# Performance work log

Measured on AMD Instinct MI355X. Metric: run time of the kernel, lower is better.

Reference implementation:

```python
import jax, jax.numpy as jnp
import numpy as np

N_NODES = 100000
N_EDGES = 1600000
IN_C, HID_C, OUT_C, K = 128, 128, 64, 3


def setup_inputs() -> dict:
    key = jax.random.key(0)
    ks = jax.random.split(key, 8)
    x = jax.random.normal(ks[0], (N_NODES, IN_C), dtype=jnp.float32)
    edge_index = jax.random.randint(ks[1], (2, N_EDGES), 0, N_NODES, dtype=jnp.int64)
    s = 0.05
    W0 = jax.random.normal(ks[2], (K, IN_C, HID_C), dtype=jnp.float32) * s
    b0 = jnp.zeros((HID_C,), dtype=jnp.float32)
    W1 = jax.random.normal(ks[3], (K, HID_C, HID_C), dtype=jnp.float32) * s
    b1 = jnp.zeros((HID_C,), dtype=jnp.float32)
    W2 = jax.random.normal(ks[4], (K, HID_C, OUT_C), dtype=jnp.float32) * s
    b2 = jnp.zeros((OUT_C,), dtype=jnp.float32)
    return {"x": x, "edge_index": edge_index, "W0": W0, "b0": b0,
            "W1": W1, "b1": b1, "W2": W2, "b2": b2}


def reference(x, edge_index, W0, b0, W1, b1, W2, b2):
    # PyG ChebConv with normalization='sym', lambda_max=2.0:
    # L_hat = L - I = -D^{-1/2} A D^{-1/2}  (self-loop weight nets to zero)
    src, dst = edge_index[0], edge_index[1]
    n = x.shape[0]
    deg = jax.ops.segment_sum(jnp.ones(src.shape, x.dtype), src, num_segments=n)
    dinv = jnp.where(deg > 0, jax.lax.rsqrt(deg), 0.0)
    w = -dinv[src] * dinv[dst]  # [E] edge weights of L_hat

    def prop(h):  # y[dst] += w * h[src]  (sparse L_hat @ h)
        return jax.ops.segment_sum(w[:, None] * h[src], dst, num_segments=n)

    def cheb_conv(h, W, b):
        # Tx_0 = h; Tx_1 = L_hat h; Tx_k = 2 L_hat Tx_{k-1} - Tx_{k-2}
        Tx0 = h
        out = Tx0 @ W[0]
        Tx1 = prop(Tx0)
        out = out + Tx1 @ W[1]
        for k in range(2, W.shape[0]):
            Tx2 = 2.0 * prop(Tx1) - Tx0
            out = out + Tx2 @ W[k]
            Tx0, Tx1 = Tx1, Tx2
        return out + b

    h = jax.nn.relu(cheb_conv(x, W0, b0))   # dropout is identity in eval mode
    h = jax.nn.relu(cheb_conv(h, W1, b1))
    return cheb_conv(h, W2, b2)
```

## Files before the change

kernel.cpp:

```cpp
#include <hip/hip_runtime.h>
#include <hip/hip_bf16.h>

#define NN 100000
#define NE 1600000
#define NB 196
#define BSH 9
#define SCH 4096

typedef _Float16 f16;
typedef __attribute__((ext_vector_type(2))) _Float16 h2;
typedef __attribute__((ext_vector_type(8))) _Float16 f16x8;
typedef __attribute__((ext_vector_type(8))) short short8;
typedef __attribute__((ext_vector_type(4))) float f32x4;

__device__ __forceinline__ short f16b(float x) {
    f16 h = (f16)x; short s; __builtin_memcpy(&s, &h, 2); return s;
}
__device__ __forceinline__ int h2i(h2 v) { int r; __builtin_memcpy(&r, &v, 4); return r; }
__device__ __forceinline__ h2 i2h(int v) { h2 r; __builtin_memcpy(&r, &v, 4); return r; }

__global__ __launch_bounds__(256) void hist_kernel(const int* __restrict__ src,
                                                   const int* __restrict__ dst,
                                                   int* __restrict__ binS,
                                                   int* __restrict__ binD, int E) {
    __shared__ int hS[NB], hD[NB];
    for (int i = threadIdx.x; i < NB; i += 256) { hS[i] = 0; hD[i] = 0; }
    __syncthreads();
    for (int e = blockIdx.x * 256 + threadIdx.x; e < E; e += gridDim.x * 256) {
        atomicAdd(&hS[src[e] >> BSH], 1);
        atomicAdd(&hD[dst[e] >> BSH], 1);
    }
    __syncthreads();
    for (int i = threadIdx.x; i < NB; i += 256) {
        if (hS[i]) atomicAdd(&binS[i], hS[i]);
        if (hD[i]) atomicAdd(&binD[i], hD[i]);
    }
}

__global__ void scan_kernel(const int* __restrict__ binS, const int* __restrict__ binD,
                            int* __restrict__ curS, int* __restrict__ offS,
                            int* __restrict__ curD, int* __restrict__ offD,
                            int* __restrict__ rowptr, int E) {
    if (threadIdx.x == 0 && blockIdx.x == 0) {
        int rs = 0, rd = 0;
        for (int i = 0; i < NB; ++i) {
            curS[i] = rs; offS[i] = rs; rs += binS[i];
            curD[i] = rd; offD[i] = rd; rd += binD[i];
        }
        offS[NB] = rs;
        offD[NB] = rd;
        rowptr[NN] = E;
    }
}

__global__ __launch_bounds__(256) void scatter_kernel(const int* __restrict__ src,
                                                      const int* __restrict__ dst,
                                                      int* __restrict__ curS,
                                                      int* __restrict__ curD,
                                                      int* __restrict__ srcB,
                                                      int* __restrict__ packB, int E) {
    __shared__ int cS[NB], cD[NB], bS[NB], bD[NB];
    int base = blockIdx.x * SCH;
    for (int i = threadIdx.x; i < NB; i += 256) { cS[i] = 0; cD[i] = 0; }
    __syncthreads();
    int s[16], d[16], rS[16], rD[16];
#pragma unroll
    for (int k = 0; k < 16; ++k) {
        int idx = base + k * 256 + threadIdx.x;
        if (idx < E) {
            s[k] = src[idx]; d[k] = dst[idx];
            rS[k] = atomicAdd(&cS[s[k] >> BSH], 1);
            rD[k] = atomicAdd(&cD[d[k] >> BSH], 1);
        } else {
            s[k] = -1;
        }
    }
    __syncthreads();
    for (int i = threadIdx.x; i < NB; i += 256) {
        if (cS[i]) bS[i] = atomicAdd(&curS[i], cS[i]);
        if (cD[i]) bD[i] = atomicAdd(&curD[i], cD[i]);
    }
    __syncthreads();
#pragma unroll
    for (int k = 0; k < 16; ++k) {
        if (s[k] >= 0) {
            srcB[bS[s[k] >> BSH] + rS[k]] = s[k];
            packB[bD[d[k] >> BSH] + rD[k]] = s[k] | ((d[k] & 511) << 20);
        }
    }
}

__global__ __launch_bounds__(256) void csr_kernel(const int* __restrict__ offD,
                                                  const int* __restrict__ packB,
                                                  int* __restrict__ rowptr,
                                                  int* __restrict__ csrCol, int n) {
    int b = blockIdx.x;
    int node0 = b << BSH;
    int nNodes = min(512, n - node0);
    if (nNodes <= 0) return;
    int beg = offD[b], end = offD[b + 1];
    __shared__ int h[512];
    __shared__ int roff[512];
    for (int i = threadIdx.x; i < 512; i += 256) h[i] = 0;
    __syncthreads();
    for (int p = beg + threadIdx.x; p < end; p += 256)
        atomicAdd(&h[(packB[p] >> 20) & 511], 1);
    __syncthreads();
    if (threadIdx.x == 0) {
        int r = beg;
        for (int i = 0; i < 512; ++i) { roff[i] = r; r += h[i]; }
    }
    __syncthreads();
    for (int i = threadIdx.x; i < nNodes; i += 256) rowptr[node0 + i] = roff[i];
    for (int i = threadIdx.x; i < 512; i += 256) h[i] = 0;
    __syncthreads();
    for (int p = beg + threadIdx.x; p < end; p += 256) {
        int pk = packB[p];
        int dl = (pk >> 20) & 511;
        int r = atomicAdd(&h[dl], 1);
        csrCol[roff[dl] + r] = pk & 0xFFFFF;
    }
}

__global__ __launch_bounds__(256) void deg_kernel(const int* __restrict__ offS,
                                                  const int* __restrict__ srcB,
                                                  float* __restrict__ dinv, int n) {
    int b = blockIdx.x;
    int node0 = b << BSH;
    int nNodes = min(512, n - node0);
    if (nNodes <= 0) return;
    int beg = offS[b], end = offS[b + 1];
    __shared__ int h[512];
    for (int i = threadIdx.x; i < 512; i += 256) h[i] = 0;
    __syncthreads();
    for (int p = beg + threadIdx.x; p < end; p += 256)
        atomicAdd(&h[srcB[p] & 511], 1);
    __syncthreads();
    for (int i = threadIdx.x; i < nNodes; i += 256) {
        int d = h[i];
        dinv[node0 + i] = d > 0 ? rsqrtf((float)d) : 0.0f;
    }
}

__global__ void convw_kernel(const float* __restrict__ W0, const float* __restrict__ W1,
                             const float* __restrict__ W2, short* __restrict__ Bt0,
                             short* __restrict__ Bt1, short* __restrict__ Bt2) {
    int i = blockIdx.x * blockDim.x + threadIdx.x;
    if (i < 49152) {
        int j = i >> 7, k = i & 127;
        int t = j >> 7, o = j & 127;
        float v = (t == 0) ? W0[k * 128 + o] - W0[2 * 16384 + k * 128 + o]
                : (t == 1) ? W0[16384 + k * 128 + o]
                           : 2.f * W0[2 * 16384 + k * 128 + o];
        Bt0[j * 128 + k] = f16b(v);
    } else if (i < 98304) {
        int m = i - 49152;
        int j = m >> 7, k = m & 127;
        int t = j >> 7, o = j & 127;
        float v = (t == 0) ? W1[k * 128 + o] - W1[2 * 16384 + k * 128 + o]
                : (t == 1) ? W1[16384 + k * 128 + o]
                           : 2.f * W1[2 * 16384 + k * 128 + o];
        Bt1[j * 128 + k] = f16b(v);
    } else if (i < 122880) {
        int m = i - 98304;
        int j = m >> 7, k = m & 127;
        int t = j >> 6, o = j & 63;
        float v = (t == 0) ? W2[k * 64 + o] - W2[2 * 8192 + k * 64 + o]
                : (t == 1) ? W2[8192 + k * 64 + o]
                           : 2.f * W2[2 * 8192 + k * 64 + o];
        Bt2[j * 128 + k] = f16b(v);
    }
}

__global__ __launch_bounds__(256) void copyx_kernel(const float* __restrict__ x,
                                                    short* __restrict__ xb, int n) {
    int i = blockIdx.x * 256 + threadIdx.x;
    if (i < n * 16) {
        const float4* xp = (const float4*)x + (size_t)i * 2;
        float4 f0 = xp[0], f1 = xp[1];
        short8 v;
        v[0] = f16b(f0.x); v[1] = f16b(f0.y); v[2] = f16b(f0.z); v[3] = f16b(f0.w);
        v[4] = f16b(f1.x); v[5] = f16b(f1.y); v[6] = f16b(f1.z); v[7] = f16b(f1.w);
        *(short8*)(xb + (size_t)i * 8) = v;
    }
}

template <int C>
__global__ __launch_bounds__(512) void gemm_kernel(const short* __restrict__ A,
                                                   const short* __restrict__ Bt,
                                                   const float* __restrict__ bias,
                                                   short* out0, short* out1, short* out2,
                                                   int n) {
    constexpr int BNT = 3 * C;
    constexpr int WC = BNT / 96;
    constexpr int WR = 8 / WC;
    constexpr int WM = 128 / WR;
    constexpr int MF = WM / 16;
    constexpr int NF = 6;
    constexpr int LDP = 40;
    constexpr int BSLOT = BNT * 4;
    constexpr int BITER = (BSLOT + 511) / 512;
    __shared__ short lds[(128 + BNT) * LDP];
    short* As = lds;
    short* Bs = lds + 128 * LDP;

    int tid = threadIdx.x;
    int lane = tid & 63;
    int wid = tid >> 6;
    int wy = wid / WC;
    int wx = wid % WC;
    int row0 = blockIdx.x * 128;
    int l15 = lane & 15;
    int kb = (lane >> 4) * 8;

    int ar = tid >> 2, aseg = tid & 3;
    int agr = row0 + ar;

    f32x4 acc[MF][NF];
#pragma unroll
    for (int i = 0; i < MF; ++i)
#pragma unroll
        for (int j = 0; j < NF; ++j) acc[i][j] = (f32x4){0.f, 0.f, 0.f, 0.f};

    short8 va;
    short8 vb[BITER];
    auto loadA = [&](int k0) {
        va = (agr < n) ? *(const short8*)(A + (size_t)agr * 128 + k0 + aseg * 8)
                       : (short8){0, 0, 0, 0, 0, 0, 0, 0};
    };
    auto loadB = [&](int k0) {
#pragma unroll
        for (int i = 0; i < BITER; ++i) {
            int slot = tid + i * 512;
            if (BSLOT % 512 == 0 || slot < BSLOT) {
                int j = slot >> 2, seg = slot & 3;
                vb[i] = *(const short8*)(Bt + (size_t)j * 128 + k0 + seg * 8);
            }
        }
    };

    loadA(0);
    loadB(0);

    for (int step = 0; step < 4; ++step) {
        *(short8*)&As[ar * LDP + aseg * 8] = va;
#pragma unroll
        for (int i = 0; i < BITER; ++i) {
            int slot = tid + i * 512;
            if (BSLOT % 512 == 0 || slot < BSLOT) {
                int j = slot >> 2, seg = slot & 3;
                *(short8*)&Bs[j * LDP + seg * 8] = vb[i];
            }
        }
        __syncthreads();
        if (step < 3) {
            loadA((step + 1) * 32);
            loadB((step + 1) * 32);
        }
        f16x8 af[MF], bfr[NF];
#pragma unroll
        for (int mf = 0; mf < MF; ++mf)
            af[mf] = *(f16x8*)&As[(wy * WM + mf * 16 + l15) * LDP + kb];
#pragma unroll
        for (int nf = 0; nf < NF; ++nf)
            bfr[nf] = *(f16x8*)&Bs[(wx * 96 + nf * 16 + l15) * LDP + kb];
#pragma unroll
        for (int mf = 0; mf < MF; ++mf)
#pragma unroll
            for (int nf = 0; nf < NF; ++nf)
                acc[mf][nf] = __builtin_amdgcn_mfma_f32_16x16x32_f16(
                    af[mf], bfr[nf], acc[mf][nf], 0, 0, 0);
        __syncthreads();
    }

    float bb[NF];
#pragma unroll
    for (int nf = 0; nf < NF; ++nf) {
        int colc = wx * 96 + nf * 16 + l15;
        bb[nf] = (colc < C) ? bias[colc] : 0.f;
    }
    short* st = lds + wid * 1536;
#pragma unroll
    for (int mf = 0; mf < MF; ++mf) {
#pragma unroll
        for (int nf = 0; nf < NF; ++nf) {
#pragma unroll
            for (int r = 0; r < 4; ++r) {
                int fr = (lane >> 4) * 4 + r;
                st[fr * 96 + nf * 16 + l15] = f16b(acc[mf][nf][r] + bb[nf]);
            }
        }
#pragma unroll
        for (int u = 0; u < 3; ++u) {
            int unit = u * 64 + lane;
            int rr = unit / 12;
            int seg = unit - rr * 12;
            int grow = row0 + wy * WM + mf * 16 + rr;
            int colc = wx * 96 + seg * 8;
            int t = colc / C, off = colc - t * C;
            short* P = (t == 0) ? out0 : (t == 1) ? out1 : out2;
            if (grow < n)
                *(int4*)&P[(size_t)grow * C + off] = *(const int4*)&st[rr * 96 + seg * 8];
        }
    }
}

template <int C, int RELU, int OUTF>
__global__ __launch_bounds__(256) void prop_kernel(const short* __restrict__ G,
                                                   const short* __restrict__ Add,
                                                   void* __restrict__ O,
                                                   const int* __restrict__ rowptr,
                                                   const int* __restrict__ csrCol,
                                                   const float* __restrict__ dinv, int n) {
    constexpr int LPE = C / 8;
    constexpr int EPG = 64 / LPE;
    constexpr int STEP = 4 * EPG;
    int wid = (blockIdx.x * blockDim.x + threadIdx.x) >> 6;
    int lane = threadIdx.x & 63;
    if (wid >= n) return;
    int beg = rowptr[wid];
    int c = rowptr[wid + 1] - beg;
    int sg = lane / LPE;
    int sl = lane & (LPE - 1);
    h2 a0 = {0, 0}, a1 = {0, 0}, a2 = {0, 0}, a3 = {0, 0};
    for (int b0 = 0; b0 < c; b0 += 64) {
        int cb = min(64, c - b0);
        int myc = 0, mywp = 0;
        if (lane < cb) {
            myc = csrCol[beg + b0 + lane];
            f16 hw = (f16)dinv[myc];
            h2 p = {hw, hw};
            mywp = h2i(p);
        }
        for (int base = 0; base < cb; base += STEP) {
            int j0 = base + sg, j1 = j0 + EPG, j2 = j0 + 2 * EPG, j3 = j0 + 3 * EPG;
            int s0 = __shfl(myc, j0);  int w0 = __shfl(mywp, j0);
            int s1 = __shfl(myc, j1);  int w1 = __shfl(mywp, j1);
            int s2 = __shfl(myc, j2);  int w2 = __shfl(mywp, j2);
            int s3 = __shfl(myc, j3);  int w3 = __shfl(mywp, j3);
            int4 v0 = *(const int4*)(G + (size_t)s0 * C + sl * 8);
            int4 v1 = *(const int4*)(G + (size_t)s1 * C + sl * 8);
            int4 v2 = *(const int4*)(G + (size_t)s2 * C + sl * 8);
            int4 v3 = *(const int4*)(G + (size_t)s3 * C + sl * 8);
            h2 p0 = i2h(w0), p1 = i2h(w1), p2 = i2h(w2), p3 = i2h(w3);
            a0 = i2h(v0.x) * p0 + a0; a1 = i2h(v0.y) * p0 + a1;
            a2 = i2h(v0.z) * p0 + a2; a3 = i2h(v0.w) * p0 + a3;
            a0 = i2h(v1.x) * p1 + a0; a1 = i2h(v1.y) * p1 + a1;
            a2 = i2h(v1.z) * p1 + a2; a3 = i2h(v1.w) * p1 + a3;
            a0 = i2h(v2.x) * p2 + a0; a1 = i2h(v2.y) * p2 + a1;
            a2 = i2h(v2.z) * p2 + a2; a3 = i2h(v2.w) * p2 + a3;
            a0 = i2h(v3.x) * p3 + a0; a1 = i2h(v3.y) * p3 + a1;
            a2 = i2h(v3.z) * p3 + a2; a3 = i2h(v3.w) * p3 + a3;
        }
    }
#pragma unroll
    for (int off = LPE; off < 64; off <<= 1) {
        a0 += i2h(__shfl_xor(h2i(a0), off));
        a1 += i2h(__shfl_xor(h2i(a1), off));
        a2 += i2h(__shfl_xor(h2i(a2), off));
        a3 += i2h(__shfl_xor(h2i(a3), off));
    }
    if (lane < LPE) {
        float scale = -dinv[wid];
        int4 ad = *(const int4*)(Add + (size_t)wid * C + sl * 8);
        h2 d0 = i2h(ad.x), d1 = i2h(ad.y), d2 = i2h(ad.z), d3 = i2h(ad.w);
        float r0 = fmaf(scale, (float)a0[0], (float)d0[0]);
        float r1 = fmaf(scale, (float)a0[1], (float)d0[1]);
        float r2 = fmaf(scale, (float)a1[0], (float)d1[0]);
        float r3 = fmaf(scale, (float)a1[1], (float)d1[1]);
        float r4 = fmaf(scale, (float)a2[0], (float)d2[0]);
        float r5 = fmaf(scale, (float)a2[1], (float)d2[1]);
        float r6 = fmaf(scale, (float)a3[0], (float)d3[0]);
        float r7 = fmaf(scale, (float)a3[1], (float)d3[1]);
        if (RELU) {
            r0 = fmaxf(r0, 0.f); r1 = fmaxf(r1, 0.f); r2 = fmaxf(r2, 0.f);
            r3 = fmaxf(r3, 0.f); r4 = fmaxf(r4, 0.f); r5 = fmaxf(r5, 0.f);
            r6 = fmaxf(r6, 0.f); r7 = fmaxf(r7, 0.f);
        }
        if (OUTF) {
            float* op = (float*)O + (size_t)wid * C + sl * 8;
            *(float4*)op = make_float4(r0, r1, r2, r3);
            *(float4*)(op + 4) = make_float4(r4, r5, r6, r7);
        } else {
            int4 w;
            h2 o0 = {(f16)r0, (f16)r1}, o1 = {(f16)r2, (f16)r3};
            h2 o2 = {(f16)r4, (f16)r5}, o3 = {(f16)r6, (f16)r7};
            w.x = h2i(o0); w.y = h2i(o1); w.z = h2i(o2); w.w = h2i(o3);
            *(int4*)((short*)O + (size_t)wid * C + sl * 8) = w;
        }
    }
}

extern "C" void kernel_launch(void* const* d_in, const int* in_sizes, int n_in,
                              void* d_out, int out_size, void* d_ws, size_t ws_size,
                              hipStream_t stream) {
    const float* x  = (const float*)d_in[0];
    const int*   ei = (const int*)d_in[1];
    const float* W0 = (const float*)d_in[2];
    const float* b0 = (const float*)d_in[3];
    const float* W1 = (const float*)d_in[4];
    const float* b1 = (const float*)d_in[5];
    const float* W2 = (const float*)d_in[6];
    const float* b2 = (const float*)d_in[7];
    float* out = (float*)d_out;

    const int n = NN, E = NE;
    const int* src = ei;
    const int* dst = ei + E;

    char* ws = (char*)d_ws;
    auto alloc = [&](size_t bytes) -> void* {
        void* p = (void*)ws;
        ws += (bytes + 255) & ~(size_t)255;
        return p;
    };
    int*   binS   = (int*)alloc(NB * 4);
    int*   binD   = (int*)alloc(NB * 4);
    int*   curS   = (int*)alloc((NB + 1) * 4);
    int*   offS   = (int*)alloc((NB + 1) * 4);
    int*   curD   = (int*)alloc((NB + 1) * 4);
    int*   offD   = (int*)alloc((NB + 1) * 4);
    int*   srcB   = (int*)alloc((size_t)E * 4);
    int*   packB  = (int*)alloc((size_t)E * 4);
    int*   rowptr = (int*)alloc((size_t)(n + 1) * 4);
    int*   csrCol = (int*)alloc((size_t)E * 4);
    float* dinv   = (float*)alloc((size_t)n * 4);
    short* xb     = (short*)alloc((size_t)n * 128 * 2);
    short* buf0   = (short*)alloc((size_t)n * 128 * 2);
    short* buf1   = (short*)alloc((size_t)n * 128 * 2);
    short* buf2   = (short*)alloc((size_t)n * 128 * 2);
    short* buf3   = (short*)alloc((size_t)n * 128 * 2);
    short* Bt0    = (short*)alloc((size_t)384 * 128 * 2);
    short* Bt1    = (short*)alloc((size_t)384 * 128 * 2);
    short* Bt2    = (short*)alloc((size_t)192 * 128 * 2);

    hipMemsetAsync(binS, 0, NB * 4, stream);
    hipMemsetAsync(binD, 0, NB * 4, stream);

    const int TPB = 256;

    hist_kernel<<<256, TPB, 0, stream>>>(src, dst, binS, binD, E);
    scan_kernel<<<1, 64, 0, stream>>>(binS, binD, curS, offS, curD, offD, rowptr, E);
    int sChunks = (E + SCH - 1) / SCH;
    scatter_kernel<<<sChunks, TPB, 0, stream>>>(src, dst, curS, curD, srcB, packB, E);
    csr_kernel<<<NB, TPB, 0, stream>>>(offD, packB, rowptr, csrCol, n);
    deg_kernel<<<NB, TPB, 0, stream>>>(offS, srcB, dinv, n);

    convw_kernel<<<(122880 + 255) / 256, 256, 0, stream>>>(W0, W1, W2, Bt0, Bt1, Bt2);
    copyx_kernel<<<(n * 16 + 255) / 256, 256, 0, stream>>>(x, xb, n);

    int pBlocks = (n + 3) / 4;
    int gBlocks = (n + 127) / 128;

    gemm_kernel<128><<<gBlocks, 512, 0, stream>>>(xb, Bt0, b0, buf0, buf1, buf2, n);
    prop_kernel<128, 0, 0><<<pBlocks, 256, 0, stream>>>(buf2, buf1, buf3, rowptr, csrCol, dinv, n);
    prop_kernel<128, 1, 0><<<pBlocks, 256, 0, stream>>>(buf3, buf0, buf1, rowptr, csrCol, dinv, n);
    gemm_kernel<128><<<gBlocks, 512, 0, stream>>>(buf1, Bt1, b1, buf0, buf1, buf2, n);
    prop_kernel<128, 0, 0><<<pBlocks, 256, 0, stream>>>(buf2, buf1, buf3, rowptr, csrCol, dinv, n);
    prop_kernel<128, 1, 0><<<pBlocks, 256, 0, stream>>>(buf3, buf0, buf1, rowptr, csrCol, dinv, n);
    gemm_kernel<64><<<gBlocks, 512, 0, stream>>>(buf1, Bt2, b2, buf0, buf3, buf2, n);
    prop_kernel<64, 0, 0><<<pBlocks, 256, 0, stream>>>(buf2, buf3, buf0 + (size_t)n * 64,
                                                       rowptr, csrCol, dinv, n);
    prop_kernel<64, 0, 1><<<pBlocks, 256, 0, stream>>>(buf0 + (size_t)n * 64, buf0, out,
                                                       rowptr, csrCol, dinv, n);
}
```

Baseline: 517.8 us.

## Slice feature buffers into column blocks and pack edge weights into CSR indices

```diff
diff --git a/kernel.cpp b/kernel.cpp
--- a/kernel.cpp
+++ b/kernel.cpp
@@ -139,6 +139,16 @@
     for (int i = threadIdx.x; i < nNodes; i += 256) {
         int d = h[i];
         dinv[node0 + i] = d > 0 ? rsqrtf((float)d) : 0.0f;
+    }
+}
+
+__global__ __launch_bounds__(256) void pk_kernel(int* __restrict__ csrCol,
+                                                 const float* __restrict__ dinv, int E) {
+    int p = blockIdx.x * 256 + threadIdx.x;
+    if (p < E) {
+        int col = csrCol[p];
+        short wb = f16b(dinv[col]);
+        csrCol[p] = (col << 15) | (wb & 0x7FFF);
     }
 }
 
@@ -174,14 +184,20 @@
 
 __global__ __launch_bounds__(256) void copyx_kernel(const float* __restrict__ x,
                                                     short* __restrict__ xb, int n) {
-    int i = blockIdx.x * 256 + threadIdx.x;
-    if (i < n * 16) {
-        const float4* xp = (const float4*)x + (size_t)i * 2;
-        float4 f0 = xp[0], f1 = xp[1];
-        short8 v;
-        v[0] = f16b(f0.x); v[1] = f16b(f0.y); v[2] = f16b(f0.z); v[3] = f16b(f0.w);
-        v[4] = f16b(f1.x); v[5] = f16b(f1.y); v[6] = f16b(f1.z); v[7] = f16b(f1.w);
-        *(short8*)(xb + (size_t)i * 8) = v;
+    int idx = blockIdx.x * 256 + threadIdx.x;
+    if (idx < 8 * n) {
+        int s = idx / NN;
+        int node = idx - s * NN;
+        const float4* xp = (const float4*)(x + (size_t)node * 128 + s * 16);
+        float4 f0 = xp[0], f1 = xp[1], f2 = xp[2], f3 = xp[3];
+        short8 v0, v1;
+        v0[0] = f16b(f0.x); v0[1] = f16b(f0.y); v0[2] = f16b(f0.z); v0[3] = f16b(f0.w);
+        v0[4] = f16b(f1.x); v0[5] = f16b(f1.y); v0[6] = f16b(f1.z); v0[7] = f16b(f1.w);
+        v1[0] = f16b(f2.x); v1[1] = f16b(f2.y); v1[2] = f16b(f2.z); v1[3] = f16b(f2.w);
+        v1[4] = f16b(f3.x); v1[5] = f16b(f3.y); v1[6] = f16b(f3.z); v1[7] = f16b(f3.w);
+        short* o = xb + (size_t)idx * 16;
+        *(short8*)o = v0;
+        *(short8*)(o + 8) = v1;
     }
 }
 
@@ -213,7 +229,9 @@
     int l15 = lane & 15;
     int kb = (lane >> 4) * 8;
 
-    int ar = tid >> 2, aseg = tid & 3;
+    int ap = tid >> 8;
+    int au = tid & 255;
+    int ar = au >> 1, ah = au & 1;
     int agr = row0 + ar;
 
     f32x4 acc[MF][NF];
@@ -225,7 +243,8 @@
     short8 va;
     short8 vb[BITER];
     auto loadA = [&](int k0) {
-        va = (agr < n) ? *(const short8*)(A + (size_t)agr * 128 + k0 + aseg * 8)
+        int s = (k0 >> 4) + ap;
+        va = (agr < n) ? *(const short8*)(A + ((size_t)s * n + agr) * 16 + ah * 8)
                        : (short8){0, 0, 0, 0, 0, 0, 0, 0};
     };
     auto loadB = [&](int k0) {
@@ -243,7 +262,7 @@
     loadB(0);
 
     for (int step = 0; step < 4; ++step) {
-        *(short8*)&As[ar * LDP + aseg * 8] = va;
+        *(short8*)&As[ar * LDP + ap * 16 + ah * 8] = va;
 #pragma unroll
         for (int i = 0; i < BITER; ++i) {
             int slot = tid + i * 512;
@@ -297,96 +316,74 @@
             int seg = unit - rr * 12;
             int grow = row0 + wy * WM + mf * 16 + rr;
             int colc = wx * 96 + seg * 8;
-            int t = colc / C, off = colc - t * C;
+            int t = colc / C, cc = colc - t * C;
             short* P = (t == 0) ? out0 : (t == 1) ? out1 : out2;
-            if (grow < n)
-                *(int4*)&P[(size_t)grow * C + off] = *(const int4*)&st[rr * 96 + seg * 8];
-        }
-    }
-}
-
-template <int C, int RELU, int OUTF>
+            if (grow < n) {
+                size_t addr;
+                if (C == 128) {
+                    int slice = cc >> 4, half = (cc >> 3) & 1;
+                    addr = ((size_t)slice * n + grow) * 16 + half * 8;
+                } else {
+                    int slice = cc >> 3;
+                    addr = ((size_t)slice * n + grow) * 8;
+                }
+                *(int4*)&P[addr] = *(const int4*)&st[rr * 96 + seg * 8];
+            }
+        }
+    }
+}
+
+template <int SW, int RELU, int OUTF>
 __global__ __launch_bounds__(256) void prop_kernel(const short* __restrict__ G,
                                                    const short* __restrict__ Add,
                                                    void* __restrict__ O,
                                                    const int* __restrict__ rowptr,
-                                                   const int* __restrict__ csrCol,
+                                                   const int* __restrict__ pkA,
                                                    const float* __restrict__ dinv, int n) {
-    constexpr int LPE = C / 8;
-    constexpr int EPG = 64 / LPE;
-    constexpr int STEP = 4 * EPG;
-    int wid = (blockIdx.x * blockDim.x + threadIdx.x) >> 6;
+    constexpr int LPN = SW / 2;
+    constexpr int NPW = 64 / LPN;
+    int slice = blockIdx.x & 7;
+    int chunk = blockIdx.x >> 3;
+    int wv = threadIdx.x >> 6;
     int lane = threadIdx.x & 63;
-    if (wid >= n) return;
-    int beg = rowptr[wid];
-    int c = rowptr[wid + 1] - beg;
-    int sg = lane / LPE;
-    int sl = lane & (LPE - 1);
-    h2 a0 = {0, 0}, a1 = {0, 0}, a2 = {0, 0}, a3 = {0, 0};
-    for (int b0 = 0; b0 < c; b0 += 64) {
-        int cb = min(64, c - b0);
-        int myc = 0, mywp = 0;
-        if (lane < cb) {
-            myc = csrCol[beg + b0 + lane];
-            f16 hw = (f16)dinv[myc];
-            h2 p = {hw, hw};
-            mywp = h2i(p);
-        }
-        for (int base = 0; base < cb; base += STEP) {
-            int j0 = base + sg, j1 = j0 + EPG, j2 = j0 + 2 * EPG, j3 = j0 + 3 * EPG;
-            int s0 = __shfl(myc, j0);  int w0 = __shfl(mywp, j0);
-            int s1 = __shfl(myc, j1);  int w1 = __shfl(mywp, j1);
-            int s2 = __shfl(myc, j2);  int w2 = __shfl(mywp, j2);
-            int s3 = __shfl(myc, j3);  int w3 = __shfl(mywp, j3);
-            int4 v0 = *(const int4*)(G + (size_t)s0 * C + sl * 8);
-            int4 v1 = *(const int4*)(G + (size_t)s1 * C + sl * 8);
-            int4 v2 = *(const int4*)(G + (size_t)s2 * C + sl * 8);
-            int4 v3 = *(const int4*)(G + (size_t)s3 * C + sl * 8);
-            h2 p0 = i2h(w0), p1 = i2h(w1), p2 = i2h(w2), p3 = i2h(w3);
-            a0 = i2h(v0.x) * p0 + a0; a1 = i2h(v0.y) * p0 + a1;
-            a2 = i2h(v0.z) * p0 + a2; a3 = i2h(v0.w) * p0 + a3;
-            a0 = i2h(v1.x) * p1 + a0; a1 = i2h(v1.y) * p1 + a1;
-            a2 = i2h(v1.z) * p1 + a2; a3 = i2h(v1.w) * p1 + a3;
-            a0 = i2h(v2.x) * p2 + a0; a1 = i2h(v2.y) * p2 + a1;
-            a2 = i2h(v2.z) * p2 + a2; a3 = i2h(v2.w) * p2 + a3;
-            a0 = i2h(v3.x) * p3 + a0; a1 = i2h(v3.y) * p3 + a1;
-            a2 = i2h(v3.z) * p3 + a2; a3 = i2h(v3.w) * p3 + a3;
-        }
-    }
-#pragma unroll
-    for (int off = LPE; off < 64; off <<= 1) {
-        a0 += i2h(__shfl_xor(h2i(a0), off));
-        a1 += i2h(__shfl_xor(h2i(a1), off));
-        a2 += i2h(__shfl_xor(h2i(a2), off));
-        a3 += i2h(__shfl_xor(h2i(a3), off));
-    }
-    if (lane < LPE) {
+    int g = lane / LPN;
+    int q = lane % LPN;
+    int wid = chunk * (4 * NPW) + wv * NPW + g;
+    bool alive = wid < n;
+    int beg = 0, cnt = 0;
+    if (alive) {
+        beg = rowptr[wid];
+        cnt = rowptr[wid + 1] - beg;
+    }
+    int mx = cnt;
+#pragma unroll
+    for (int off = 32; off >= 1; off >>= 1) mx = max(mx, __shfl_xor(mx, off));
+
+    const short* Gs = G + (size_t)slice * n * SW;
+    h2 acc = {0, 0};
+    for (int j = 0; j < mx; ++j) {
+        if (j < cnt) {
+            int p = pkA[beg + j];
+            unsigned col = ((unsigned)p) >> 15;
+            int wb = p & 0x7FFF;
+            h2 w = i2h(wb | (wb << 16));
+            int v = *(const int*)(Gs + (size_t)col * SW + q * 2);
+            acc = i2h(v) * w + acc;
+        }
+    }
+    if (alive) {
         float scale = -dinv[wid];
-        int4 ad = *(const int4*)(Add + (size_t)wid * C + sl * 8);
-        h2 d0 = i2h(ad.x), d1 = i2h(ad.y), d2 = i2h(ad.z), d3 = i2h(ad.w);
-        float r0 = fmaf(scale, (float)a0[0], (float)d0[0]);
-        float r1 = fmaf(scale, (float)a0[1], (float)d0[1]);
-        float r2 = fmaf(scale, (float)a1[0], (float)d1[0]);
-        float r3 = fmaf(scale, (float)a1[1], (float)d1[1]);
-        float r4 = fmaf(scale, (float)a2[0], (float)d2[0]);
-        float r5 = fmaf(scale, (float)a2[1], (float)d2[1]);
-        float r6 = fmaf(scale, (float)a3[0], (float)d3[0]);
-        float r7 = fmaf(scale, (float)a3[1], (float)d3[1]);
-        if (RELU) {
-            r0 = fmaxf(r0, 0.f); r1 = fmaxf(r1, 0.f); r2 = fmaxf(r2, 0.f);
-            r3 = fmaxf(r3, 0.f); r4 = fmaxf(r4, 0.f); r5 = fmaxf(r5, 0.f);
-            r6 = fmaxf(r6, 0.f); r7 = fmaxf(r7, 0.f);
-        }
+        int ad = *(const int*)(Add + ((size_t)slice * n + wid) * SW + q * 2);
+        h2 a = i2h(ad);
+        float r0 = fmaf(scale, (float)acc[0], (float)a[0]);
+        float r1 = fmaf(scale, (float)acc[1], (float)a[1]);
+        if (RELU) { r0 = fmaxf(r0, 0.f); r1 = fmaxf(r1, 0.f); }
         if (OUTF) {
-            float* op = (float*)O + (size_t)wid * C + sl * 8;
-            *(float4*)op = make_float4(r0, r1, r2, r3);
-            *(float4*)(op + 4) = make_float4(r4, r5, r6, r7);
+            float* op = (float*)O + (size_t)wid * 64 + slice * SW + q * 2;
+            op[0] = r0; op[1] = r1;
         } else {
-            int4 w;
-            h2 o0 = {(f16)r0, (f16)r1}, o1 = {(f16)r2, (f16)r3};
-            h2 o2 = {(f16)r4, (f16)r5}, o3 = {(f16)r6, (f16)r7};
-            w.x = h2i(o0); w.y = h2i(o1); w.z = h2i(o2); w.w = h2i(o3);
-            *(int4*)((short*)O + (size_t)wid * C + sl * 8) = w;
+            h2 o = {(f16)r0, (f16)r1};
+            *(int*)((short*)O + ((size_t)slice * n + wid) * SW + q * 2) = h2i(o);
         }
     }
 }
@@ -445,22 +442,24 @@
     scatter_kernel<<<sChunks, TPB, 0, stream>>>(src, dst, curS, curD, srcB, packB, E);
     csr_kernel<<<NB, TPB, 0, stream>>>(offD, packB, rowptr, csrCol, n);
     deg_kernel<<<NB, TPB, 0, stream>>>(offS, srcB, dinv, n);
+    pk_kernel<<<(E + 255) / 256, 256, 0, stream>>>(csrCol, dinv, E);
 
     convw_kernel<<<(122880 + 255) / 256, 256, 0, stream>>>(W0, W1, W2, Bt0, Bt1, Bt2);
-    copyx_kernel<<<(n * 16 + 255) / 256, 256, 0, stream>>>(x, xb, n);
-
-    int pBlocks = (n + 3) / 4;
+    copyx_kernel<<<(8 * n + 255) / 256, 256, 0, stream>>>(x, xb, n);
+
     int gBlocks = (n + 127) / 128;
+    int p16Blocks = ((n + 31) / 32) * 8;
+    int p8Blocks  = ((n + 63) / 64) * 8;
 
     gemm_kernel<128><<<gBlocks, 512, 0, stream>>>(xb, Bt0, b0, buf0, buf1, buf2, n);
-    prop_kernel<128, 0, 0><<<pBlocks, 256, 0, stream>>>(buf2, buf1, buf3, rowptr, csrCol, dinv, n);
-    prop_kernel<128, 1, 0><<<pBlocks, 256, 0, stream>>>(buf3, buf0, buf1, rowptr, csrCol, dinv, n);
+    prop_kernel<16, 0, 0><<<p16Blocks, 256, 0, stream>>>(buf2, buf1, buf3, rowptr, csrCol, dinv, n);
+    prop_kernel<16, 1, 0><<<p16Blocks, 256, 0, stream>>>(buf3, buf0, buf1, rowptr, csrCol, dinv, n);
     gemm_kernel<128><<<gBlocks, 512, 0, stream>>>(buf1, Bt1, b1, buf0, buf1, buf2, n);
-    prop_kernel<128, 0, 0><<<pBlocks, 256, 0, stream>>>(buf2, buf1, buf3, rowptr, csrCol, dinv, n);
-    prop_kernel<128, 1, 0><<<pBlocks, 256, 0, stream>>>(buf3, buf0, buf1, rowptr, csrCol, dinv, n);
+    prop_kernel<16, 0, 0><<<p16Blocks, 256, 0, stream>>>(buf2, buf1, buf3, rowptr, csrCol, dinv, n);
+    prop_kernel<16, 1, 0><<<p16Blocks, 256, 0, stream>>>(buf3, buf0, buf1, rowptr, csrCol, dinv, n);
     gemm_kernel<64><<<gBlocks, 512, 0, stream>>>(buf1, Bt2, b2, buf0, buf3, buf2, n);
-    prop_kernel<64, 0, 0><<<pBlocks, 256, 0, stream>>>(buf2, buf3, buf0 + (size_t)n * 64,
+    prop_kernel<8, 0, 0><<<p8Blocks, 256, 0, stream>>>(buf2, buf3, buf0 + (size_t)n * 64,
                                                        rowptr, csrCol, dinv, n);
-    prop_kernel<64, 0, 1><<<pBlocks, 256, 0, stream>>>(buf0 + (size_t)n * 64, buf0, out,
+    prop_kernel<8, 0, 1><<<p8Blocks, 256, 0, stream>>>(buf0 + (size_t)n * 64, buf0, out,
                                                        rowptr, csrCol, dinv, n);
 }
```

Result: slower. 1.110 ms (+114.4%).

## Shrink GEMM tile to 64 rows with 256 threads and drop register prefetch

Applied to the files above, without the earlier changes.

```diff
diff --git a/kernel.cpp b/kernel.cpp
--- a/kernel.cpp
+++ b/kernel.cpp
@@ -186,30 +186,30 @@
 }
 
 template <int C>
-__global__ __launch_bounds__(512) void gemm_kernel(const short* __restrict__ A,
+__global__ __launch_bounds__(256) void gemm_kernel(const short* __restrict__ A,
                                                    const short* __restrict__ Bt,
                                                    const float* __restrict__ bias,
                                                    short* out0, short* out1, short* out2,
                                                    int n) {
     constexpr int BNT = 3 * C;
     constexpr int WC = BNT / 96;
-    constexpr int WR = 8 / WC;
-    constexpr int WM = 128 / WR;
+    constexpr int WR = 4 / WC;
+    constexpr int WM = 64 / WR;
     constexpr int MF = WM / 16;
     constexpr int NF = 6;
     constexpr int LDP = 40;
     constexpr int BSLOT = BNT * 4;
-    constexpr int BITER = (BSLOT + 511) / 512;
-    __shared__ short lds[(128 + BNT) * LDP];
+    constexpr int BITER = BSLOT / 256;
+    __shared__ short lds[(64 + BNT) * LDP];
     short* As = lds;
-    short* Bs = lds + 128 * LDP;
+    short* Bs = lds + 64 * LDP;
 
     int tid = threadIdx.x;
     int lane = tid & 63;
     int wid = tid >> 6;
     int wy = wid / WC;
     int wx = wid % WC;
-    int row0 = blockIdx.x * 128;
+    int row0 = blockIdx.x * 64;
     int l15 = lane & 15;
     int kb = (lane >> 4) * 8;
 
@@ -222,41 +222,20 @@
 #pragma unroll
         for (int j = 0; j < NF; ++j) acc[i][j] = (f32x4){0.f, 0.f, 0.f, 0.f};
 
-    short8 va;
-    short8 vb[BITER];
-    auto loadA = [&](int k0) {
-        va = (agr < n) ? *(const short8*)(A + (size_t)agr * 128 + k0 + aseg * 8)
-                       : (short8){0, 0, 0, 0, 0, 0, 0, 0};
-    };
-    auto loadB = [&](int k0) {
+    for (int step = 0; step < 4; ++step) {
+        int k0 = step * 32;
+        short8 va = (agr < n)
+            ? *(const short8*)(A + (size_t)agr * 128 + k0 + aseg * 8)
+            : (short8){0, 0, 0, 0, 0, 0, 0, 0};
+        *(short8*)&As[ar * LDP + aseg * 8] = va;
 #pragma unroll
         for (int i = 0; i < BITER; ++i) {
-            int slot = tid + i * 512;
-            if (BSLOT % 512 == 0 || slot < BSLOT) {
-                int j = slot >> 2, seg = slot & 3;
-                vb[i] = *(const short8*)(Bt + (size_t)j * 128 + k0 + seg * 8);
-            }
-        }
-    };
-
-    loadA(0);
-    loadB(0);
-
-    for (int step = 0; step < 4; ++step) {
-        *(short8*)&As[ar * LDP + aseg * 8] = va;
-#pragma unroll
-        for (int i = 0; i < BITER; ++i) {
-            int slot = tid + i * 512;
-            if (BSLOT % 512 == 0 || slot < BSLOT) {
-                int j = slot >> 2, seg = slot & 3;
-                *(short8*)&Bs[j * LDP + seg * 8] = vb[i];
-            }
+            int slot = tid + i * 256;
+            int j = slot >> 2, seg = slot & 3;
+            *(short8*)&Bs[j * LDP + seg * 8] =
+                *(const short8*)(Bt + (size_t)j * 128 + k0 + seg * 8);
         }
         __syncthreads();
-        if (step < 3) {
-            loadA((step + 1) * 32);
-            loadB((step + 1) * 32);
-        }
         f16x8 af[MF], bfr[NF];
 #pragma unroll
         for (int mf = 0; mf < MF; ++mf)
@@ -450,15 +429,15 @@
     copyx_kernel<<<(n * 16 + 255) / 256, 256, 0, stream>>>(x, xb, n);
 
     int pBlocks = (n + 3) / 4;
-    int gBlocks = (n + 127) / 128;
-
-    gemm_kernel<128><<<gBlocks, 512, 0, stream>>>(xb, Bt0, b0, buf0, buf1, buf2, n);
+    int gBlocks = (n + 63) / 64;
+
+    gemm_kernel<128><<<gBlocks, 256, 0, stream>>>(xb, Bt0, b0, buf0, buf1, buf2, n);
     prop_kernel<128, 0, 0><<<pBlocks, 256, 0, stream>>>(buf2, buf1, buf3, rowptr, csrCol, dinv, n);
     prop_kernel<128, 1, 0><<<pBlocks, 256, 0, stream>>>(buf3, buf0, buf1, rowptr, csrCol, dinv, n);
-    gemm_kernel<128><<<gBlocks, 512, 0, stream>>>(buf1, Bt1, b1, buf0, buf1, buf2, n);
+    gemm_kernel<128><<<gBlocks, 256, 0, stream>>>(buf1, Bt1, b1, buf0, buf1, buf2, n);
     prop_kernel<128, 0, 0><<<pBlocks, 256, 0, stream>>>(buf2, buf1, buf3, rowptr, csrCol, dinv, n);
     prop_kernel<128, 1, 0><<<pBlocks, 256, 0, stream>>>(buf3, buf0, buf1, rowptr, csrCol, dinv, n);
-    gemm_kernel<64><<<gBlocks, 512, 0, stream>>>(buf1, Bt2, b2, buf0, buf3, buf2, n);
+    gemm_kernel<64><<<gBlocks, 256, 0, stream>>>(buf1, Bt2, b2, buf0, buf3, buf2, n);
     prop_kernel<64, 0, 0><<<pBlocks, 256, 0, stream>>>(buf2, buf3, buf0 + (size_t)n * 64,
                                                        rowptr, csrCol, dinv, n);
     prop_kernel<64, 0, 1><<<pBlocks, 256, 0, stream>>>(buf0 + (size_t)n * 64, buf0, out,
```

Result: no change. 518.5 us (+0.1%).
